# Kernel optimization log

Measured on AMD Instinct MI355X. Metric: run time of the kernel, lower is better.

The kernel has to match this reference:

```python
import jax, jax.numpy as jnp
import numpy as np

RETRIEVE_TEMP = 1.0
USAGE_SCALE = 0.5
CONF_SCALE = 0.5
SIG_SCALE = 1.0


def _l2norm(x, axis=-1, eps=1e-12):
    # matches torch F.normalize: x / max(||x||, eps)
    n = jnp.sqrt(jnp.sum(x * x, axis=axis, keepdims=True))
    return x / jnp.maximum(n, eps)


def setup_inputs() -> dict:
    key = jax.random.key(0)
    ks = jax.random.split(key, 7)
    N, T, U, B, S, R = 4, 2048, 64, 64, 128, 256
    q_u = jax.random.uniform(ks[0], (N, T, U), dtype=jnp.float32)
    q_b = jax.random.uniform(ks[1], (N, T, B), dtype=jnp.float32)
    q_sigma = jax.random.normal(ks[2], (N, T, S), dtype=jnp.float32)
    delta_rule_proto = jax.random.normal(ks[3], (U, B, R), dtype=jnp.float32)
    signature_proto = jax.random.normal(ks[4], (U, B, S), dtype=jnp.float32)
    # ~half of the cells have zero write mass so the validity mask is exercised
    write_mass = jnp.maximum(jax.random.uniform(ks[5], (U, B), dtype=jnp.float32) * 2.0 - 1.0, 0.0)
    ema_conf = jax.random.uniform(ks[6], (U, B), dtype=jnp.float32)
    return {"q_u": q_u, "q_b": q_b, "q_sigma": q_sigma,
            "delta_rule_proto": delta_rule_proto, "signature_proto": signature_proto,
            "write_mass": write_mass, "ema_conf": ema_conf}


def reference(q_u, q_b, q_sigma, delta_rule_proto, signature_proto, write_mass, ema_conf):
    # joint prob over (operator u, binding v): [n,t,u,v]
    joint = q_u[..., :, None] * q_b[..., None, :]
    valid = (write_mass > 0).astype(joint.dtype)            # [u,v]
    joint_logit = jnp.log(jnp.maximum(joint, 1e-6))

    usage_prior = jnp.log1p(write_mass)
    usage_prior = usage_prior / jnp.maximum(usage_prior.max(), 1.0)
    conf_prior = ema_conf / jnp.maximum(ema_conf.max(), 1e-6)

    qs = _l2norm(q_sigma)
    sp = _l2norm(signature_proto + 1e-6)
    sig_score = jnp.einsum('nts,uvs->ntuv', qs, sp)
    sig_score = 0.5 * (1.0 + sig_score)

    logits = (joint_logit + USAGE_SCALE * usage_prior + CONF_SCALE * conf_prior
              + SIG_SCALE * sig_score)                       # [n,t,u,v]

    batch_shape = logits.shape[:-2]
    UV = logits.shape[-2] * logits.shape[-1]
    flat_logits = logits.reshape(*batch_shape, UV)
    flat_valid = valid.reshape(UV)
    masked = jnp.where(flat_valid > 0, flat_logits, jnp.float32(-1e9))
    w = jax.nn.softmax(masked / RETRIEVE_TEMP, axis=-1)
    w = w * flat_valid
    w = w / jnp.maximum(jnp.sum(w, axis=-1, keepdims=True), 1e-6)  # [n,t,UV]

    weights = w.reshape(logits.shape)                        # [n,t,u,v]
    memory_delta_rule = jnp.einsum('ntuv,uvr->ntr', weights, delta_rule_proto)
    memory_signature = jnp.einsum('ntuv,uvs->nts', weights, signature_proto)

    flat_sig = sig_score.reshape(*batch_shape, UV)
    flat_conf = conf_prior.reshape(UV)
    top_index = jnp.argmax(w, axis=-1)                       # [n,t]
    top_weight = jnp.take_along_axis(w, top_index[..., None], axis=-1)
    top_conf = flat_conf[top_index][..., None]
    top_sig = jnp.take_along_axis(flat_sig, top_index[..., None], axis=-1)
    memory_conf = jnp.clip(top_weight * top_conf * top_sig, 0.0, 1.0)

    return (memory_delta_rule, memory_signature, memory_conf, weights, top_weight)
```

## Files before the change

kernel.cpp:

```cpp
#include <hip/hip_runtime.h>
#include <math.h>

#define NT   8192
#define UV   4096
#define SDIM 128
#define LOG1EM6 -13.815510557964274f

#define O_DELTA 0
#define O_SIG   2097152
#define O_CONF  3145728
#define O_W     3153920
#define O_TOPW  36708352

#define W_K4P   0
#define W_QSHI  0
#define W_QSLO  524288
#define W_SPHI  1048576
#define W_SPLO  1310720
#define W_LQU   1572864
#define W_LQB   2097152
#define W_BIAS  2621440
#define W_CONFN 2625536
#define W_VALID 2629632
#define W_PSUM  2633728
#define W_PMAX  2895872
#define W_PSIG  3158016
#define W_PUV   3420160
#define W_RINV  3682304
#define W_PTHI  3690496
#define W_PTLO  4476928

typedef __attribute__((ext_vector_type(8))) short short8;
typedef __attribute__((ext_vector_type(4))) float floatx4;

__device__ __forceinline__ unsigned short f2bf(float x) {
    unsigned u = __builtin_bit_cast(unsigned, x);
    u = u + 0x7fffu + ((u >> 16) & 1u);
    return (unsigned short)(u >> 16);
}
__device__ __forceinline__ float bf2f(unsigned short h) {
    unsigned u = ((unsigned)h) << 16;
    return __builtin_bit_cast(float, u);
}

__device__ __forceinline__ void gload_lds16(const void* g, void* l) {
    __builtin_amdgcn_global_load_lds(
        (const __attribute__((address_space(1))) unsigned*)g,
        (__attribute__((address_space(3))) unsigned*)l, 16, 0, 0);
}

__global__ __launch_bounds__(256)
void kprep(const float* __restrict__ qu, const float* __restrict__ qb,
           const float* __restrict__ qsig, const float* __restrict__ drp,
           const float* __restrict__ spr, const float* __restrict__ wm,
           const float* __restrict__ ec, float* __restrict__ ws)
{
    __shared__ float red1[256];
    __shared__ float red2[256];
    __shared__ float tile[32][33];

    const int bid = blockIdx.x;
    const int tid = threadIdx.x;

    if (bid < 3072) {
        const int wid  = bid * 4 + (tid >> 6);
        const int lane = tid & 63;
        if (wid < UV) {
            const float* src = spr + (size_t)wid * SDIM;
            float a = src[lane] + 1e-6f;
            float b = src[lane + 64] + 1e-6f;
            float ss = a * a + b * b;
            for (int m = 32; m > 0; m >>= 1) ss += __shfl_xor(ss, m);
            float inv = 1.0f / fmaxf(sqrtf(ss), 1e-12f);
            a *= inv; b *= inv;
            unsigned short* hi = (unsigned short*)(ws + W_SPHI);
            unsigned short* lo = (unsigned short*)(ws + W_SPLO);
            unsigned short ha = f2bf(a), hb = f2bf(b);
            hi[wid * 128 + lane]      = ha;
            hi[wid * 128 + lane + 64] = hb;
            lo[wid * 128 + lane]      = f2bf(a - bf2f(ha));
            lo[wid * 128 + lane + 64] = f2bf(b - bf2f(hb));
        } else {
            const int row = wid - UV;
            const float* src = qsig + (size_t)row * SDIM;
            float a = src[lane];
            float b = src[lane + 64];
            float ss = a * a + b * b;
            for (int m = 32; m > 0; m >>= 1) ss += __shfl_xor(ss, m);
            float inv = 1.0f / fmaxf(sqrtf(ss), 1e-12f);
            a *= inv; b *= inv;
            unsigned short* hi = (unsigned short*)(ws + W_QSHI);
            unsigned short* lo = (unsigned short*)(ws + W_QSLO);
            unsigned short ha = f2bf(a), hb = f2bf(b);
            hi[row * 128 + lane]      = ha;
            hi[row * 128 + lane + 64] = hb;
            lo[row * 128 + lane]      = f2bf(a - bf2f(ha));
            lo[row * 128 + lane + 64] = f2bf(b - bf2f(hb));
        }
    } else if (bid < 4608) {
        const int sub = bid - 3072;
        const int k0  = (sub & 127) * 32;
        const int n0  = (sub >> 7) * 32;
        {
            const int kr = tid >> 3, nc = (tid & 7) * 4;
            const int n = n0 + nc;
            float4 v;
            if (n < 256) v = *(const float4*)&drp[(size_t)(k0 + kr) * 256 + n];
            else         v = *(const float4*)&spr[(size_t)(k0 + kr) * 128 + (n - 256)];
            tile[kr][nc] = v.x; tile[kr][nc + 1] = v.y;
            tile[kr][nc + 2] = v.z; tile[kr][nc + 3] = v.w;
        }
        __syncthreads();
        {
            const int nr = tid >> 3, kc = (tid & 7) * 4;
            unsigned short* pth = (unsigned short*)(ws + W_PTHI);
            unsigned short* ptl = (unsigned short*)(ws + W_PTLO);
            ushort4 h, l;
            float x;
            x = tile[kc + 0][nr]; h.x = f2bf(x); l.x = f2bf(x - bf2f(h.x));
            x = tile[kc + 1][nr]; h.y = f2bf(x); l.y = f2bf(x - bf2f(h.y));
            x = tile[kc + 2][nr]; h.z = f2bf(x); l.z = f2bf(x - bf2f(h.z));
            x = tile[kc + 3][nr]; h.w = f2bf(x); l.w = f2bf(x - bf2f(h.w));
            *(ushort4*)&pth[(size_t)(n0 + nr) * 4096 + k0 + kc] = h;
            *(ushort4*)&ptl[(size_t)(n0 + nr) * 4096 + k0 + kc] = l;
        }
    } else if (bid < 5632) {
        const int sub = bid - 4608;
        const int t = (sub & 511) * 256 + tid;
        const float* src = (sub >> 9) ? qb : qu;
        float* dst = ws + ((sub >> 9) ? W_LQB : W_LQU);
        float4 v = *(const float4*)&src[t * 4];
        v.x = __logf(v.x); v.y = __logf(v.y);
        v.z = __logf(v.z); v.w = __logf(v.w);
        *(float4*)&dst[t * 4] = v;
    } else {
        float m1 = 0.0f, m2 = 0.0f;
        for (int i = tid; i < UV; i += 256) {
            m1 = fmaxf(m1, log1pf(wm[i]));
            m2 = fmaxf(m2, ec[i]);
        }
        red1[tid] = m1; red2[tid] = m2;
        __syncthreads();
        for (int s = 128; s > 0; s >>= 1) {
            if (tid < s) {
                red1[tid] = fmaxf(red1[tid], red1[tid + s]);
                red2[tid] = fmaxf(red2[tid], red2[tid + s]);
            }
            __syncthreads();
        }
        const float inv1 = 1.0f / fmaxf(red1[0], 1.0f);
        const float inv2 = 1.0f / fmaxf(red2[0], 1e-6f);
        for (int i = tid; i < UV; i += 256) {
            float w  = wm[i];
            float un = log1pf(w) * inv1;
            float cn = ec[i] * inv2;
            ws[W_BIAS  + i] = 0.5f * un + 0.5f * cn;
            ws[W_CONFN + i] = cn;
            ws[W_VALID + i] = (w > 0.0f) ? 1.0f : 0.0f;
        }
    }
}

#define SA3 40

__global__ __launch_bounds__(256, 4)
void k3_mfma(float* __restrict__ ws, float* __restrict__ dout)
{
    __shared__ unsigned short sAh[64 * SA3];
    __shared__ unsigned short sAl[64 * SA3];
    __shared__ unsigned short sBh[128 * SA3];
    __shared__ unsigned short sBl[128 * SA3];
    __shared__ float sS[2][64], sM[2][64], sG[2][64], sU[2][64];

    const int tid  = threadIdx.x;
    const int row0 = blockIdx.x * 64;
    const int cb   = blockIdx.y;
    const int n0   = cb * 128;

    const unsigned short* qsh = (const unsigned short*)(ws + W_QSHI);
    const unsigned short* qsl = (const unsigned short*)(ws + W_QSLO);
    const unsigned short* sph = (const unsigned short*)(ws + W_SPHI);
    const unsigned short* spl = (const unsigned short*)(ws + W_SPLO);

    const int tAr = tid >> 2;
    const int tAk = (tid & 3) * 8;
    const int tBn = tid >> 2;
    const int tBk = (tid & 3) * 8;

    uint4 pah, pal, pbh[2], pbl[2];
    {
        pah = *(const uint4*)&qsh[(size_t)(row0 + tAr) * 128 + tAk];
        pal = *(const uint4*)&qsl[(size_t)(row0 + tAr) * 128 + tAk];
        #pragma unroll
        for (int p = 0; p < 2; ++p) {
            pbh[p] = *(const uint4*)&sph[(size_t)(n0 + tBn + p * 64) * 128 + tBk];
            pbl[p] = *(const uint4*)&spl[(size_t)(n0 + tBn + p * 64) * 128 + tBk];
        }
    }

    const int lane = tid & 63;
    const int wid  = tid >> 6;
    const int wm   = wid & 1;
    const int wn   = wid >> 1;
    const int fr   = lane & 15;
    const int fq   = lane >> 4;
    const int ako  = fq * 8;

    floatx4 acc[2][4];
    #pragma unroll
    for (int mt = 0; mt < 2; ++mt)
        #pragma unroll
        for (int nt = 0; nt < 4; ++nt)
            acc[mt][nt] = (floatx4){0.f, 0.f, 0.f, 0.f};

    for (int kc = 0; kc < 4; ++kc) {
        __syncthreads();
        *(uint4*)&sAh[tAr * SA3 + tAk] = pah;
        *(uint4*)&sAl[tAr * SA3 + tAk] = pal;
        #pragma unroll
        for (int p = 0; p < 2; ++p) {
            *(uint4*)&sBh[(tBn + p * 64) * SA3 + tBk] = pbh[p];
            *(uint4*)&sBl[(tBn + p * 64) * SA3 + tBk] = pbl[p];
        }
        __syncthreads();

        if (kc < 3) {
            const int kn = (kc + 1) * 32;
            pah = *(const uint4*)&qsh[(size_t)(row0 + tAr) * 128 + kn + tAk];
            pal = *(const uint4*)&qsl[(size_t)(row0 + tAr) * 128 + kn + tAk];
            #pragma unroll
            for (int p = 0; p < 2; ++p) {
                pbh[p] = *(const uint4*)&sph[(size_t)(n0 + tBn + p * 64) * 128 + kn + tBk];
                pbl[p] = *(const uint4*)&spl[(size_t)(n0 + tBn + p * 64) * 128 + kn + tBk];
            }
        }

        short8 afh[2], afl[2], bfh[4], bfl[4];
        #pragma unroll
        for (int mt = 0; mt < 2; ++mt) {
            const int m = wm * 32 + mt * 16 + fr;
            afh[mt] = *(const short8*)&sAh[m * SA3 + ako];
            afl[mt] = *(const short8*)&sAl[m * SA3 + ako];
        }
        #pragma unroll
        for (int nt = 0; nt < 4; ++nt) {
            const int n = wn * 64 + nt * 16 + fr;
            bfh[nt] = *(const short8*)&sBh[n * SA3 + ako];
            bfl[nt] = *(const short8*)&sBl[n * SA3 + ako];
        }
        #pragma unroll
        for (int mt = 0; mt < 2; ++mt)
            #pragma unroll
            for (int nt = 0; nt < 4; ++nt)
                acc[mt][nt] = __builtin_amdgcn_mfma_f32_16x16x32_bf16(
                    afh[mt], bfh[nt], acc[mt][nt], 0, 0, 0);
        #pragma unroll
        for (int mt = 0; mt < 2; ++mt)
            #pragma unroll
            for (int nt = 0; nt < 4; ++nt)
                acc[mt][nt] = __builtin_amdgcn_mfma_f32_16x16x32_bf16(
                    afh[mt], bfl[nt], acc[mt][nt], 0, 0, 0);
        #pragma unroll
        for (int mt = 0; mt < 2; ++mt)
            #pragma unroll
            for (int nt = 0; nt < 4; ++nt)
                acc[mt][nt] = __builtin_amdgcn_mfma_f32_16x16x32_bf16(
                    afl[mt], bfh[nt], acc[mt][nt], 0, 0, 0);
    }

    const float* lqu    = ws + W_LQU;
    const float* lqb    = ws + W_LQB;
    const float* bias   = ws + W_BIAS;
    const float* validf = ws + W_VALID;
    float* wout = dout + O_W;

    float ps[2][4], pm[2][4], pg[2][4], pu[2][4];
    #pragma unroll
    for (int mt = 0; mt < 2; ++mt)
        #pragma unroll
        for (int r = 0; r < 4; ++r) {
            ps[mt][r] = 0.f; pm[mt][r] = -1e30f; pg[mt][r] = 0.f; pu[mt][r] = 0.f;
        }

    #pragma unroll
    for (int mt = 0; mt < 2; ++mt) {
        const int rbase = row0 + wm * 32 + mt * 16 + fq * 4;
        #pragma unroll
        for (int nt = 0; nt < 4; ++nt) {
            const int uvb = n0 + wn * 64 + nt * 16;
            const int u   = uvb >> 6;
            const int uv  = uvb + fr;
            const int v   = uv & 63;
            const float bv = bias[uv];
            const float vd = validf[uv];
            const floatx4 a = acc[mt][nt];
            #pragma unroll
            for (int reg = 0; reg < 4; ++reg) {
                const int row = rbase + reg;
                const float jl  = fmaxf(lqu[(row << 6) + u] + lqb[(row << 6) + v], LOG1EM6);
                const float sig = fmaf(0.5f, a[reg], 0.5f);
                const float lg  = jl + bv + sig;
                const float e   = (vd > 0.f) ? __expf(lg - 2.f) : 0.f;
                wout[((size_t)row << 12) + uv] = e;
                ps[mt][reg] += e;
                if (vd > 0.f && lg > pm[mt][reg]) {
                    pm[mt][reg] = lg; pu[mt][reg] = (float)uv; pg[mt][reg] = sig;
                }
            }
        }
    }

    #pragma unroll
    for (int off = 1; off < 16; off <<= 1) {
        #pragma unroll
        for (int mt = 0; mt < 2; ++mt)
            #pragma unroll
            for (int r = 0; r < 4; ++r) {
                ps[mt][r] += __shfl_xor(ps[mt][r], off);
                float om = __shfl_xor(pm[mt][r], off);
                float ou = __shfl_xor(pu[mt][r], off);
                float og = __shfl_xor(pg[mt][r], off);
                if (om > pm[mt][r] || (om == pm[mt][r] && ou < pu[mt][r])) {
                    pm[mt][r] = om; pu[mt][r] = ou; pg[mt][r] = og;
                }
            }
    }
    if (fr == 0) {
        #pragma unroll
        for (int mt = 0; mt < 2; ++mt)
            #pragma unroll
            for (int r = 0; r < 4; ++r) {
                const int rl = wm * 32 + mt * 16 + fq * 4 + r;
                sS[wn][rl] = ps[mt][r]; sM[wn][rl] = pm[mt][r];
                sG[wn][rl] = pg[mt][r]; sU[wn][rl] = pu[mt][r];
            }
    }
    __syncthreads();
    if (tid < 64) {
        const float s  = sS[0][tid] + sS[1][tid];
        const float m0 = sM[0][tid], m1 = sM[1][tid];
        float m, uvf, g;
        if (m0 > m1 || (m0 == m1 && sU[0][tid] <= sU[1][tid])) {
            m = m0; uvf = sU[0][tid]; g = sG[0][tid];
        } else {
            m = m1; uvf = sU[1][tid]; g = sG[1][tid];
        }
        const int row = row0 + tid;
        ws[W_PSUM + cb * NT + row] = s;
        ws[W_PMAX + cb * NT + row] = m;
        ws[W_PSIG + cb * NT + row] = g;
        ws[W_PUV  + cb * NT + row] = uvf;
    }
}

__global__ __launch_bounds__(256)
void k3b_stats(float* __restrict__ ws, float* __restrict__ dout)
{
    const int row = blockIdx.x * 256 + threadIdx.x;
    float s = 0.f, m = -1e30f, uvf = 0.f, g = 0.f;
    for (int cb = 0; cb < 32; ++cb) {
        s += ws[W_PSUM + cb * NT + row];
        const float om = ws[W_PMAX + cb * NT + row];
        const float ou = ws[W_PUV  + cb * NT + row];
        const float og = ws[W_PSIG + cb * NT + row];
        if (om > m || (om == m && ou < uvf)) { m = om; uvf = ou; g = og; }
    }
    const float inv = 1.0f / s;
    ws[W_RINV + row] = inv;
    const float topw = __expf(m - 2.f) * inv;
    dout[O_TOPW + row] = topw;
    const int uvi = (int)uvf;
    const float cf = topw * ws[W_CONFN + uvi] * g;
    dout[O_CONF + row] = fminf(fmaxf(cf, 0.f), 1.f);
}

__global__ __launch_bounds__(512, 1)
void k4_mfma(float* __restrict__ ws, float* __restrict__ dout)
{
    __shared__ unsigned short sB[2][2][12288];

    const int tid  = threadIdx.x;
    const int lane = tid & 63;
    const int wv   = tid >> 6;

    const int bid = blockIdx.x;
    const int xcd = bid & 7;
    const int ks  = xcd >> 2;
    const int rt  = ((bid >> 3) << 2) | (xcd & 3);
    const int row0 = rt * 64;
    const int kb   = ks * 2048;

    const unsigned short* pth = (const unsigned short*)(ws + W_PTHI);
    const unsigned short* ptl = (const unsigned short*)(ws + W_PTLO);

    int st_pl[6], st_ubase[6], st_goff[6];
    #pragma unroll
    for (int j = 0; j < 6; ++j) {
        const int cu = (tid & ~63) + j * 512;
        const int c  = cu + lane;
        const int pl = (cu >= 1536) ? 1 : 0;
        const int cc = c - pl * 1536;
        const int col = cc >> 2;
        const int sl  = (cc & 3) ^ ((col >> 1) & 3);
        st_pl[j]    = pl;
        st_ubase[j] = pl * 24576 + (cu - pl * 1536) * 16;
        st_goff[j]  = col * UV + sl * 8;
    }

    const int fr = lane & 15;
    const int fq = lane >> 4;

    const int wm = wv & 3;
    const int wn = wv >> 2;

    const int arow = row0 + wm * 16 + fr;
    const float* aptr = dout + O_W + (size_t)arow * UV + kb + fq * 8;
    float*       awb  = dout + O_W + (size_t)arow * UV + kb + fq * 8;
    const float rinv_a = ws[W_RINV + arow];

    int boff[12];
    #pragma unroll
    for (int nt = 0; nt < 12; ++nt) {
        const int col = wn * 192 + nt * 16 + fr;
        boff[nt] = col * 32 + ((fq ^ ((col >> 1) & 3)) * 8);
    }

    floatx4 acc[12];
    #pragma unroll
    for (int nt = 0; nt < 12; ++nt)
        acc[nt] = (floatx4){0.f, 0.f, 0.f, 0.f};

    auto stage = [&](int kc_, int buf_) {
        const int kk = kb + kc_ * 32;
        #pragma unroll
        for (int j = 0; j < 6; ++j) {
            const unsigned short* src = (st_pl[j] ? ptl : pth) + st_goff[j] + kk;
            char* dst = (char*)(&sB[buf_][0][0]) + st_ubase[j];
            gload_lds16(src, dst);
        }
    };

    stage(0, 0);
    float4 a0 = *(const float4*)(aptr);
    float4 a1 = *(const float4*)(aptr + 4);
    __syncthreads();

    float4 p0 = {}, p1 = {};
    int buf = 0;
    for (int kc = 0; kc < 64; ++kc) {
        float4 n0 = {}, n1 = {};
        if (kc + 1 < 64) {
            stage(kc + 1, buf ^ 1);
            n0 = *(const float4*)(aptr + (size_t)(kc + 1) * 32);
            n1 = *(const float4*)(aptr + (size_t)(kc + 1) * 32 + 4);
        }

        if (wn == 0 && kc > 0) {
            float4 w0, w1;
            w0.x = p0.x * rinv_a; w0.y = p0.y * rinv_a;
            w0.z = p0.z * rinv_a; w0.w = p0.w * rinv_a;
            w1.x = p1.x * rinv_a; w1.y = p1.y * rinv_a;
            w1.z = p1.z * rinv_a; w1.w = p1.w * rinv_a;
            *(float4*)(awb + (size_t)(kc - 1) * 32)     = w0;
            *(float4*)(awb + (size_t)(kc - 1) * 32 + 4) = w1;
        }

        short8 afh, afl;
        {
            const float f[8] = {a0.x, a0.y, a0.z, a0.w, a1.x, a1.y, a1.z, a1.w};
            #pragma unroll
            for (int j = 0; j < 8; ++j) {
                const unsigned short h = f2bf(f[j]);
                afh[j] = (short)h;
                afl[j] = (short)f2bf(f[j] - bf2f(h));
            }
        }

        const unsigned short* bh = &sB[buf][0][0];
        const unsigned short* bl = &sB[buf][1][0];
        #pragma unroll
        for (int nt = 0; nt < 12; ++nt) {
            const short8 bfh = *(const short8*)&bh[boff[nt]];
            const short8 bfl = *(const short8*)&bl[boff[nt]];
            acc[nt] = __builtin_amdgcn_mfma_f32_16x16x32_bf16(afh, bfh, acc[nt], 0, 0, 0);
            acc[nt] = __builtin_amdgcn_mfma_f32_16x16x32_bf16(afh, bfl, acc[nt], 0, 0, 0);
            acc[nt] = __builtin_amdgcn_mfma_f32_16x16x32_bf16(afl, bfh, acc[nt], 0, 0, 0);
        }

        p0 = a0; p1 = a1;
        __syncthreads();
        a0 = n0; a1 = n1;
        buf ^= 1;
    }
    if (wn == 0) {
        float4 w0, w1;
        w0.x = p0.x * rinv_a; w0.y = p0.y * rinv_a;
        w0.z = p0.z * rinv_a; w0.w = p0.w * rinv_a;
        w1.x = p1.x * rinv_a; w1.y = p1.y * rinv_a;
        w1.z = p1.z * rinv_a; w1.w = p1.w * rinv_a;
        *(float4*)(awb + (size_t)63 * 32)     = w0;
        *(float4*)(awb + (size_t)63 * 32 + 4) = w1;
    }

    const int gr = row0 + wm * 16 + fq * 4;
    float rv[4];
    #pragma unroll
    for (int r = 0; r < 4; ++r) rv[r] = ws[W_RINV + gr + r];

    #pragma unroll
    for (int nt = 0; nt < 12; ++nt) {
        const int gc = wn * 192 + nt * 16 + fr;
        floatx4 a = acc[nt];
        a[0] *= rv[0]; a[1] *= rv[1]; a[2] *= rv[2]; a[3] *= rv[3];
        if (ks == 0) {
            if (gc < 256) {
                float* o = dout + O_DELTA;
                o[(size_t)(gr + 0) * 256 + gc] = a[0];
                o[(size_t)(gr + 1) * 256 + gc] = a[1];
                o[(size_t)(gr + 2) * 256 + gc] = a[2];
                o[(size_t)(gr + 3) * 256 + gc] = a[3];
            } else {
                float* o = dout + O_SIG;
                const int c = gc - 256;
                o[(size_t)(gr + 0) * 128 + c] = a[0];
                o[(size_t)(gr + 1) * 128 + c] = a[1];
                o[(size_t)(gr + 2) * 128 + c] = a[2];
                o[(size_t)(gr + 3) * 128 + c] = a[3];
            }
        } else {
            float* p = ws + W_K4P;
            p[(size_t)(gr + 0) * 384 + gc] = a[0];
            p[(size_t)(gr + 1) * 384 + gc] = a[1];
            p[(size_t)(gr + 2) * 384 + gc] = a[2];
            p[(size_t)(gr + 3) * 384 + gc] = a[3];
        }
    }
}

__global__ __launch_bounds__(256)
void k4b_reduce(const float* __restrict__ ws, float* __restrict__ dout)
{
    const int idx = blockIdx.x * 256 + threadIdx.x;
    const int row = idx / 96;
    const int c   = (idx - row * 96) * 4;
    const float4 p = *(const float4*)&ws[W_K4P + (size_t)row * 384 + c];
    float* dst = (c < 256) ? (dout + O_DELTA + (size_t)row * 256 + c)
                           : (dout + O_SIG   + (size_t)row * 128 + (c - 256));
    float4 d = *(float4*)dst;
    d.x += p.x; d.y += p.y; d.z += p.z; d.w += p.w;
    *(float4*)dst = d;
}

extern "C" void kernel_launch(void* const* d_in, const int* in_sizes, int n_in,
                              void* d_out, int out_size, void* d_ws, size_t ws_size,
                              hipStream_t stream)
{
    const float* qu   = (const float*)d_in[0];
    const float* qb   = (const float*)d_in[1];
    const float* qsig = (const float*)d_in[2];
    const float* drp  = (const float*)d_in[3];
    const float* spr  = (const float*)d_in[4];
    const float* wm   = (const float*)d_in[5];
    const float* ec   = (const float*)d_in[6];
    float* out = (float*)d_out;
    float* ws  = (float*)d_ws;

    kprep<<<5633, 256, 0, stream>>>(qu, qb, qsig, drp, spr, wm, ec, ws);
    k3_mfma<<<dim3(128, 32), 256, 0, stream>>>(ws, out);
    k3b_stats<<<32, 256, 0, stream>>>(ws, out);
    k4_mfma<<<256, 512, 0, stream>>>(ws, out);
    k4b_reduce<<<3072, 256, 0, stream>>>(ws, out);
}
```

Before: 426.4 us.

## Triple-buffer k4 B-tile staging with explicit vmcnt waits and one barrier

After: 451.5 us. 5.9% more time.

```diff
diff --git a/kernel.cpp b/kernel.cpp
--- a/kernel.cpp
+++ b/kernel.cpp
@@ -377,7 +377,7 @@
 __global__ __launch_bounds__(512, 1)
 void k4_mfma(float* __restrict__ ws, float* __restrict__ dout)
 {
-    __shared__ unsigned short sB[2][2][12288];
+    __shared__ unsigned short sB[3][2][12288];
 
     const int tid  = threadIdx.x;
     const int lane = tid & 63;
@@ -440,19 +440,31 @@
         }
     };
 
+    float4 a0x, a0y, a1x, a1y, a2x, a2y, p0, p1;
     stage(0, 0);
-    float4 a0 = *(const float4*)(aptr);
-    float4 a1 = *(const float4*)(aptr + 4);
-    __syncthreads();
-
-    float4 p0 = {}, p1 = {};
-    int buf = 0;
+    a0x = *(const float4*)(aptr);
+    a0y = *(const float4*)(aptr + 4);
+    stage(1, 1);
+    a1x = *(const float4*)(aptr + 32);
+    a1y = *(const float4*)(aptr + 32 + 4);
+    p0 = (float4){}; p1 = (float4){};
+
     for (int kc = 0; kc < 64; ++kc) {
-        float4 n0 = {}, n1 = {};
-        if (kc + 1 < 64) {
-            stage(kc + 1, buf ^ 1);
-            n0 = *(const float4*)(aptr + (size_t)(kc + 1) * 32);
-            n1 = *(const float4*)(aptr + (size_t)(kc + 1) * 32 + 4);
+        if (kc < 63) {
+            asm volatile("s_waitcnt vmcnt(8)" ::: "memory");
+        } else {
+            asm volatile("s_waitcnt vmcnt(0)" ::: "memory");
+        }
+        __builtin_amdgcn_sched_barrier(0);
+        __builtin_amdgcn_s_barrier();
+        __builtin_amdgcn_sched_barrier(0);
+
+        if (kc + 2 < 64) {
+            stage(kc + 2, (kc + 2) % 3);
+            a2x = *(const float4*)(aptr + (size_t)(kc + 2) * 32);
+            a2y = *(const float4*)(aptr + (size_t)(kc + 2) * 32 + 4);
+        } else {
+            a2x = (float4){}; a2y = (float4){};
         }
 
         if (wn == 0 && kc > 0) {
@@ -467,7 +479,8 @@
 
         short8 afh, afl;
         {
-            const float f[8] = {a0.x, a0.y, a0.z, a0.w, a1.x, a1.y, a1.z, a1.w};
+            const float f[8] = {a0x.x, a0x.y, a0x.z, a0x.w,
+                                a0y.x, a0y.y, a0y.z, a0y.w};
             #pragma unroll
             for (int j = 0; j < 8; ++j) {
                 const unsigned short h = f2bf(f[j]);
@@ -476,8 +489,8 @@
             }
         }
 
-        const unsigned short* bh = &sB[buf][0][0];
-        const unsigned short* bl = &sB[buf][1][0];
+        const unsigned short* bh = &sB[kc % 3][0][0];
+        const unsigned short* bl = &sB[kc % 3][1][0];
         #pragma unroll
         for (int nt = 0; nt < 12; ++nt) {
             const short8 bfh = *(const short8*)&bh[boff[nt]];
@@ -487,10 +500,9 @@
             acc[nt] = __builtin_amdgcn_mfma_f32_16x16x32_bf16(afl, bfh, acc[nt], 0, 0, 0);
         }
 
-        p0 = a0; p1 = a1;
-        __syncthreads();
-        a0 = n0; a1 = n1;
-        buf ^= 1;
+        p0 = a0x; p1 = a0y;
+        a0x = a1x; a0y = a1y;
+        a1x = a2x; a1y = a2y;
     }
     if (wn == 0) {
         float4 w0, w1;
```

## Switch k4 GEMM to 32x32x16 MFMA tiles with two k-subslices per stage

Applied to the files above, without the earlier changes.

Result: slower. 484.3 us (+13.6%).

```diff
diff --git a/kernel.cpp b/kernel.cpp
--- a/kernel.cpp
+++ b/kernel.cpp
@@ -32,6 +32,7 @@
 
 typedef __attribute__((ext_vector_type(8))) short short8;
 typedef __attribute__((ext_vector_type(4))) float floatx4;
+typedef __attribute__((ext_vector_type(16))) float floatx16;
 
 __device__ __forceinline__ unsigned short f2bf(float x) {
     unsigned u = __builtin_bit_cast(unsigned, x);
@@ -377,7 +378,7 @@
 __global__ __launch_bounds__(512, 1)
 void k4_mfma(float* __restrict__ ws, float* __restrict__ dout)
 {
-    __shared__ unsigned short sB[2][2][12288];
+    __shared__ __align__(16) unsigned short sB[2][2][12288];
 
     const int tid  = threadIdx.x;
     const int lane = tid & 63;
@@ -393,146 +394,156 @@
     const unsigned short* pth = (const unsigned short*)(ws + W_PTHI);
     const unsigned short* ptl = (const unsigned short*)(ws + W_PTLO);
 
-    int st_pl[6], st_ubase[6], st_goff[6];
+    int st_pl[6], st_lbase[6], st_goff[6];
     #pragma unroll
     for (int j = 0; j < 6; ++j) {
         const int cu = (tid & ~63) + j * 512;
         const int c  = cu + lane;
-        const int pl = (cu >= 1536) ? 1 : 0;
+        const int pl = (c >= 1536) ? 1 : 0;
         const int cc = c - pl * 1536;
         const int col = cc >> 2;
-        const int sl  = (cc & 3) ^ ((col >> 1) & 3);
+        const int slot = cc & 3;
         st_pl[j]    = pl;
-        st_ubase[j] = pl * 24576 + (cu - pl * 1536) * 16;
-        st_goff[j]  = col * UV + sl * 8;
-    }
-
-    const int fr = lane & 15;
-    const int fq = lane >> 4;
-
-    const int wm = wv & 3;
-    const int wn = wv >> 2;
-
-    const int arow = row0 + wm * 16 + fr;
-    const float* aptr = dout + O_W + (size_t)arow * UV + kb + fq * 8;
-    float*       awb  = dout + O_W + (size_t)arow * UV + kb + fq * 8;
+        st_lbase[j] = pl * 24576 + (cu - pl * 1536) * 16;
+        st_goff[j]  = col * UV + ((slot ^ ((col >> 1) & 3)) * 8);
+    }
+
+    const int cl = lane & 31;
+    const int h  = lane >> 5;
+    const int wm = wv & 1;
+    const int wn = wv >> 1;
+
+    const int arow = row0 + wm * 32 + cl;
+    const float* aptr = dout + O_W + (size_t)arow * UV + kb + h * 8;
+    float*       awb  = dout + O_W + (size_t)arow * UV + kb + h * 8;
     const float rinv_a = ws[W_RINV + arow];
 
-    int boff[12];
-    #pragma unroll
-    for (int nt = 0; nt < 12; ++nt) {
-        const int col = wn * 192 + nt * 16 + fr;
-        boff[nt] = col * 32 + ((fq ^ ((col >> 1) & 3)) * 8);
-    }
-
-    floatx4 acc[12];
-    #pragma unroll
-    for (int nt = 0; nt < 12; ++nt)
-        acc[nt] = (floatx4){0.f, 0.f, 0.f, 0.f};
+    int boff[3][2];
+    #pragma unroll
+    for (int nt = 0; nt < 3; ++nt) {
+        const int colL = wn * 96 + nt * 32 + cl;
+        const int g = (colL >> 1) & 3;
+        #pragma unroll
+        for (int ksub = 0; ksub < 2; ++ksub)
+            boff[nt][ksub] = colL * 64 + ((((ksub << 1) | h) ^ g) << 4);
+    }
+
+    floatx16 acc[3];
+    #pragma unroll
+    for (int nt = 0; nt < 3; ++nt)
+        #pragma unroll
+        for (int i = 0; i < 16; ++i) acc[nt][i] = 0.f;
 
     auto stage = [&](int kc_, int buf_) {
         const int kk = kb + kc_ * 32;
         #pragma unroll
         for (int j = 0; j < 6; ++j) {
             const unsigned short* src = (st_pl[j] ? ptl : pth) + st_goff[j] + kk;
-            char* dst = (char*)(&sB[buf_][0][0]) + st_ubase[j];
+            char* dst = (char*)(&sB[0][0][0]) + buf_ * 49152 + st_lbase[j];
             gload_lds16(src, dst);
         }
     };
 
     stage(0, 0);
-    float4 a0 = *(const float4*)(aptr);
+    float4 a0 = *(const float4*)(aptr + 0);
     float4 a1 = *(const float4*)(aptr + 4);
+    float4 a2 = *(const float4*)(aptr + 16);
+    float4 a3 = *(const float4*)(aptr + 20);
     __syncthreads();
 
-    float4 p0 = {}, p1 = {};
-    int buf = 0;
+    float4 p0 = (float4){}, p1 = (float4){}, p2 = (float4){}, p3 = (float4){};
     for (int kc = 0; kc < 64; ++kc) {
-        float4 n0 = {}, n1 = {};
+        float4 n0 = (float4){}, n1 = (float4){}, n2 = (float4){}, n3 = (float4){};
         if (kc + 1 < 64) {
-            stage(kc + 1, buf ^ 1);
-            n0 = *(const float4*)(aptr + (size_t)(kc + 1) * 32);
-            n1 = *(const float4*)(aptr + (size_t)(kc + 1) * 32 + 4);
+            stage(kc + 1, (kc + 1) & 1);
+            const size_t ko = (size_t)(kc + 1) * 32;
+            n0 = *(const float4*)(aptr + ko);
+            n1 = *(const float4*)(aptr + ko + 4);
+            n2 = *(const float4*)(aptr + ko + 16);
+            n3 = *(const float4*)(aptr + ko + 20);
         }
 
         if (wn == 0 && kc > 0) {
-            float4 w0, w1;
-            w0.x = p0.x * rinv_a; w0.y = p0.y * rinv_a;
-            w0.z = p0.z * rinv_a; w0.w = p0.w * rinv_a;
-            w1.x = p1.x * rinv_a; w1.y = p1.y * rinv_a;
-            w1.z = p1.z * rinv_a; w1.w = p1.w * rinv_a;
-            *(float4*)(awb + (size_t)(kc - 1) * 32)     = w0;
-            *(float4*)(awb + (size_t)(kc - 1) * 32 + 4) = w1;
-        }
-
-        short8 afh, afl;
-        {
-            const float f[8] = {a0.x, a0.y, a0.z, a0.w, a1.x, a1.y, a1.z, a1.w};
-            #pragma unroll
-            for (int j = 0; j < 8; ++j) {
-                const unsigned short h = f2bf(f[j]);
-                afh[j] = (short)h;
-                afl[j] = (short)f2bf(f[j] - bf2f(h));
-            }
-        }
-
-        const unsigned short* bh = &sB[buf][0][0];
-        const unsigned short* bl = &sB[buf][1][0];
-        #pragma unroll
-        for (int nt = 0; nt < 12; ++nt) {
-            const short8 bfh = *(const short8*)&bh[boff[nt]];
-            const short8 bfl = *(const short8*)&bl[boff[nt]];
-            acc[nt] = __builtin_amdgcn_mfma_f32_16x16x32_bf16(afh, bfh, acc[nt], 0, 0, 0);
-            acc[nt] = __builtin_amdgcn_mfma_f32_16x16x32_bf16(afh, bfl, acc[nt], 0, 0, 0);
-            acc[nt] = __builtin_amdgcn_mfma_f32_16x16x32_bf16(afl, bfh, acc[nt], 0, 0, 0);
-        }
-
-        p0 = a0; p1 = a1;
+            const size_t wo = (size_t)(kc - 1) * 32;
+            float4 w;
+            w.x = p0.x * rinv_a; w.y = p0.y * rinv_a; w.z = p0.z * rinv_a; w.w = p0.w * rinv_a;
+            *(float4*)(awb + wo) = w;
+            w.x = p1.x * rinv_a; w.y = p1.y * rinv_a; w.z = p1.z * rinv_a; w.w = p1.w * rinv_a;
+            *(float4*)(awb + wo + 4) = w;
+            w.x = p2.x * rinv_a; w.y = p2.y * rinv_a; w.z = p2.z * rinv_a; w.w = p2.w * rinv_a;
+            *(float4*)(awb + wo + 16) = w;
+            w.x = p3.x * rinv_a; w.y = p3.y * rinv_a; w.z = p3.z * rinv_a; w.w = p3.w * rinv_a;
+            *(float4*)(awb + wo + 20) = w;
+        }
+
+        const char* bb = (const char*)(&sB[0][0][0]) + (kc & 1) * 49152;
+        #pragma unroll
+        for (int ksub = 0; ksub < 2; ++ksub) {
+            short8 afh, afl;
+            {
+                const float4 u = ksub ? a2 : a0;
+                const float4 v = ksub ? a3 : a1;
+                const float f[8] = {u.x, u.y, u.z, u.w, v.x, v.y, v.z, v.w};
+                #pragma unroll
+                for (int j = 0; j < 8; ++j) {
+                    const unsigned short hh = f2bf(f[j]);
+                    afh[j] = (short)hh;
+                    afl[j] = (short)f2bf(f[j] - bf2f(hh));
+                }
+            }
+            short8 bfh[3], bfl[3];
+            #pragma unroll
+            for (int nt = 0; nt < 3; ++nt) {
+                bfh[nt] = *(const short8*)(bb + boff[nt][ksub]);
+                bfl[nt] = *(const short8*)(bb + 24576 + boff[nt][ksub]);
+            }
+            #pragma unroll
+            for (int nt = 0; nt < 3; ++nt)
+                acc[nt] = __builtin_amdgcn_mfma_f32_32x32x16_bf16(afh, bfh[nt], acc[nt], 0, 0, 0);
+            #pragma unroll
+            for (int nt = 0; nt < 3; ++nt)
+                acc[nt] = __builtin_amdgcn_mfma_f32_32x32x16_bf16(afh, bfl[nt], acc[nt], 0, 0, 0);
+            #pragma unroll
+            for (int nt = 0; nt < 3; ++nt)
+                acc[nt] = __builtin_amdgcn_mfma_f32_32x32x16_bf16(afl, bfh[nt], acc[nt], 0, 0, 0);
+        }
+
         __syncthreads();
-        a0 = n0; a1 = n1;
-        buf ^= 1;
+        p0 = a0; p1 = a1; p2 = a2; p3 = a3;
+        a0 = n0; a1 = n1; a2 = n2; a3 = n3;
     }
     if (wn == 0) {
-        float4 w0, w1;
-        w0.x = p0.x * rinv_a; w0.y = p0.y * rinv_a;
-        w0.z = p0.z * rinv_a; w0.w = p0.w * rinv_a;
-        w1.x = p1.x * rinv_a; w1.y = p1.y * rinv_a;
-        w1.z = p1.z * rinv_a; w1.w = p1.w * rinv_a;
-        *(float4*)(awb + (size_t)63 * 32)     = w0;
-        *(float4*)(awb + (size_t)63 * 32 + 4) = w1;
-    }
-
-    const int gr = row0 + wm * 16 + fq * 4;
-    float rv[4];
-    #pragma unroll
-    for (int r = 0; r < 4; ++r) rv[r] = ws[W_RINV + gr + r];
-
-    #pragma unroll
-    for (int nt = 0; nt < 12; ++nt) {
-        const int gc = wn * 192 + nt * 16 + fr;
-        floatx4 a = acc[nt];
-        a[0] *= rv[0]; a[1] *= rv[1]; a[2] *= rv[2]; a[3] *= rv[3];
-        if (ks == 0) {
-            if (gc < 256) {
-                float* o = dout + O_DELTA;
-                o[(size_t)(gr + 0) * 256 + gc] = a[0];
-                o[(size_t)(gr + 1) * 256 + gc] = a[1];
-                o[(size_t)(gr + 2) * 256 + gc] = a[2];
-                o[(size_t)(gr + 3) * 256 + gc] = a[3];
+        const size_t wo = (size_t)63 * 32;
+        float4 w;
+        w.x = p0.x * rinv_a; w.y = p0.y * rinv_a; w.z = p0.z * rinv_a; w.w = p0.w * rinv_a;
+        *(float4*)(awb + wo) = w;
+        w.x = p1.x * rinv_a; w.y = p1.y * rinv_a; w.z = p1.z * rinv_a; w.w = p1.w * rinv_a;
+        *(float4*)(awb + wo + 4) = w;
+        w.x = p2.x * rinv_a; w.y = p2.y * rinv_a; w.z = p2.z * rinv_a; w.w = p2.w * rinv_a;
+        *(float4*)(awb + wo + 16) = w;
+        w.x = p3.x * rinv_a; w.y = p3.y * rinv_a; w.z = p3.z * rinv_a; w.w = p3.w * rinv_a;
+        *(float4*)(awb + wo + 20) = w;
+    }
+
+    const int rbase = row0 + wm * 32 + 4 * h;
+    float rv[16];
+    #pragma unroll
+    for (int reg = 0; reg < 16; ++reg)
+        rv[reg] = ws[W_RINV + rbase + (reg & 3) + 8 * (reg >> 2)];
+
+    #pragma unroll
+    for (int nt = 0; nt < 3; ++nt) {
+        const int gc = wn * 96 + nt * 32 + cl;
+        #pragma unroll
+        for (int reg = 0; reg < 16; ++reg) {
+            const int gr = rbase + (reg & 3) + 8 * (reg >> 2);
+            const float v = acc[nt][reg] * rv[reg];
+            if (ks == 0) {
+                if (gc < 256) dout[O_DELTA + (size_t)gr * 256 + gc] = v;
+                else          dout[O_SIG   + (size_t)gr * 128 + (gc - 256)] = v;
             } else {
-                float* o = dout + O_SIG;
-                const int c = gc - 256;
-                o[(size_t)(gr + 0) * 128 + c] = a[0];
-                o[(size_t)(gr + 1) * 128 + c] = a[1];
-                o[(size_t)(gr + 2) * 128 + c] = a[2];
-                o[(size_t)(gr + 3) * 128 + c] = a[3];
-            }
-        } else {
-            float* p = ws + W_K4P;
-            p[(size_t)(gr + 0) * 384 + gc] = a[0];
-            p[(size_t)(gr + 1) * 384 + gc] = a[1];
-            p[(size_t)(gr + 2) * 384 + gc] = a[2];
-            p[(size_t)(gr + 3) * 384 + gc] = a[3];
+                ws[W_K4P + (size_t)gr * 384 + gc] = v;
+            }
         }
     }
 }
```
